# Kernel tuning notes

Hardware: AMD Instinct MI355X
Metric: run time of the kernel (lower is better)

Reference implementation:

```python
import jax, jax.numpy as jnp
import numpy as np

H = 8      # heads
D = 64     # dim_head
N0 = 1024  # modality-0 tokens
N1 = 1024  # modality-1 tokens
N = N0 + N1  # == token_num
DI = H * D   # dim_inner = 512


def setup_inputs() -> dict:
    key = jax.random.key(0)
    ks = jax.random.split(key, 10)
    s = 0.02
    return {
        "x0": jax.random.normal(ks[0], (1, N0, 512), jnp.float32),
        "x1": jax.random.normal(ks[1], (1, N1, 512), jnp.float32),
        "mask0": jnp.ones((1, N0), jnp.bool_),
        "mask1": jnp.ones((1, N1), jnp.bool_),
        "attn_dist": jax.random.normal(ks[2], (1, N, N), jnp.float32),
        "W_in0": jax.random.normal(ks[3], (512, 3 * DI), jnp.float32) * s,
        "W_in1": jax.random.normal(ks[4], (512, 3 * DI), jnp.float32) * s,
        "W_tau": jax.random.normal(ks[5], (DI, N * H), jnp.float32) * s,
        "b_tau": jax.random.normal(ks[6], (N * H,), jnp.float32) * s,
        "W_out0": jax.random.normal(ks[7], (DI, 512), jnp.float32) * s,
        "W_out1": jax.random.normal(ks[8], (DI, 512), jnp.float32) * s,
    }


def _split_heads(qkv, B, n):
    # (B, n, 3*H*D) -> (3, B, H, n, D)   [matches Rearrange 'b n (qkv h d) -> qkv b h n d']
    return qkv.reshape(B, n, 3, H, D).transpose(2, 0, 3, 1, 4)


def reference(x0, x1, mask0, mask1, attn_dist, W_in0, W_in1, W_tau, b_tau, W_out0, W_out1):
    B = x0.shape[0]
    qkv0 = _split_heads(x0 @ W_in0, B, N0)
    qkv1 = _split_heads(x1 @ W_in1, B, N1)
    qkv = jnp.concatenate([qkv0, qkv1], axis=3)  # pack along token axis -> (3,B,H,N,D)
    q, k, v = qkv[0], qkv[1], qkv[2]
    mask = jnp.concatenate([mask0, mask1], axis=1)  # (B, N)

    sim = jnp.einsum('bhid,bhjd->bhij', q, k) / jnp.sqrt(jnp.array(D, q.dtype))
    neg = -jnp.finfo(sim.dtype).max
    sim = jnp.where(mask[:, None, None, :], sim, neg)

    # taus: raw row-major reshape of q (B,H,N,D) -> (B,N,H*D), as in torch .reshape
    q_flat = q.reshape(B, N, H * D)
    taus = (q_flat @ W_tau + b_tau).reshape(B, N, N, H)
    bias = (taus * attn_dist[..., None]).transpose(0, 3, 1, 2)  # (B,H,N,N)
    sim = sim - bias

    attn = jax.nn.softmax(sim.astype(jnp.float32), axis=-1).astype(sim.dtype)
    out = jnp.einsum('bhij,bhjd->bhid', attn, v)
    out = out.transpose(0, 2, 1, 3).reshape(B, N, H * D)  # merge heads

    out0 = out[:, :N0] @ W_out0
    out1 = out[:, N0:] @ W_out1
    return (out0, out1)
```

## Files before the change

### kernel.cpp

```cpp
#include <hip/hip_runtime.h>
#include <stdint.h>

typedef __bf16 bf16;
typedef __bf16 bf16x8 __attribute__((ext_vector_type(8)));
typedef float f32x4 __attribute__((ext_vector_type(4)));
typedef unsigned short u16x8 __attribute__((ext_vector_type(8)));

#define MFMA16(a, b, c) __builtin_amdgcn_mfma_f32_16x16x32_bf16(a, b, c, 0, 0, 0)

static __device__ __forceinline__ bf16x8 lds_frag(const unsigned short* p) {
  return __builtin_bit_cast(bf16x8, *(const u16x8*)p);
}

static __device__ __forceinline__ bf16x8 gmem_frag(const bf16* p) {
  return __builtin_bit_cast(bf16x8, *(const u16x8*)p);
}

static __device__ __forceinline__ u16x8 cvt8(const float* p) {
  f32x4 a = *(const f32x4*)p;
  f32x4 b = *(const f32x4*)(p + 4);
  u16x8 r;
#pragma unroll
  for (int e = 0; e < 4; ++e) {
    r[e] = __builtin_bit_cast(unsigned short, (bf16)a[e]);
    r[4 + e] = __builtin_bit_cast(unsigned short, (bf16)b[e]);
  }
  return r;
}

__global__ __launch_bounds__(256) void prep_kernel(
    const float* __restrict__ Wti, const float* __restrict__ btau,
    const float* __restrict__ x0, const float* __restrict__ x1,
    const float* __restrict__ Win0, const float* __restrict__ Win1,
    const float* __restrict__ Wo0, const float* __restrict__ Wo1,
    bf16* __restrict__ Wto, float* __restrict__ bto, bf16* __restrict__ xb,
    bf16* __restrict__ Winb0, bf16* __restrict__ Winb1,
    bf16* __restrict__ Wob0, bf16* __restrict__ Wob1) {
  const int b = blockIdx.x;
  const int tid = threadIdx.x;
  __shared__ unsigned short shm[8 * 32 * 72];

  if (b < 512) {
    const int c0 = (b & 7) * 64;
    const int j0 = (b >> 3) * 32;
#pragma unroll
    for (int it = 0; it < 8; ++it) {
      int idx = it * 256 + tid;
      int c = idx >> 5, j = idx & 31;
      u16x8 v = cvt8(Wti + (size_t)(c0 + c) * 16384 + (j0 + j) * 8);
#pragma unroll
      for (int h = 0; h < 8; ++h) shm[(h * 32 + j) * 72 + c] = v[h];
    }
    __syncthreads();
#pragma unroll
    for (int it = 0; it < 8; ++it) {
      int chunk = it * 256 + tid;
      int row = chunk >> 3, ck = chunk & 7;
      int h = row >> 5, j = row & 31;
      u16x8 v = *(const u16x8*)&shm[row * 72 + ck * 8];
      *(u16x8*)((unsigned short*)Wto + (size_t)(h * 2048 + j0 + j) * 512 + c0 + ck * 8) = v;
    }
    if ((b & 7) == 0) {
      int j = tid >> 3, h = tid & 7;
      bto[h * 2048 + j0 + j] = btau[(j0 + j) * 8 + h];
    }
  } else if (b < 896) {
    int t = b - 512;
    const float* W = t < 192 ? Win0 : Win1;
    bf16* Wb = t < 192 ? Winb0 : Winb1;
    t = t < 192 ? t : t - 192;
    const int c0 = (t & 7) * 64, n0 = (t >> 3) * 64;
#pragma unroll
    for (int it = 0; it < 2; ++it) {
      int idx = it * 256 + tid;
      int c = idx >> 3, nn = idx & 7;
      u16x8 v = cvt8(W + (size_t)(c0 + c) * 1536 + n0 + nn * 8);
#pragma unroll
      for (int e = 0; e < 8; ++e) shm[(nn * 8 + e) * 72 + c] = v[e];
    }
    __syncthreads();
#pragma unroll
    for (int it = 0; it < 2; ++it) {
      int idx = it * 256 + tid;
      int n = idx >> 3, ck = idx & 7;
      *(u16x8*)((unsigned short*)Wb + (size_t)(n0 + n) * 512 + c0 + ck * 8) =
          *(const u16x8*)&shm[n * 72 + ck * 8];
    }
  } else if (b < 1408) {
    int t = b - 896;
    const float* src = t < 256 ? x0 : x1;
    size_t dst0 = t < 256 ? 0 : 524288;
    int tt = t < 256 ? t : t - 256;
    size_t off = (size_t)tt * 2048 + tid * 8;
    u16x8 v = cvt8(src + off);
    *(u16x8*)((unsigned short*)xb + dst0 + off) = v;
  } else {
    int t = b - 1408;
    const float* W = t < 64 ? Wo0 : Wo1;
    bf16* Wb = t < 64 ? Wob0 : Wob1;
    t &= 63;
    const int c0 = (t & 7) * 64, n0 = (t >> 3) * 64;
#pragma unroll
    for (int it = 0; it < 2; ++it) {
      int idx = it * 256 + tid;
      int c = idx >> 3, nn = idx & 7;
      u16x8 v = cvt8(W + (size_t)(c0 + c) * 512 + n0 + nn * 8);
#pragma unroll
      for (int e = 0; e < 8; ++e) shm[(nn * 8 + e) * 72 + c] = v[e];
    }
    __syncthreads();
#pragma unroll
    for (int it = 0; it < 2; ++it) {
      int idx = it * 256 + tid;
      int n = idx >> 3, ck = idx & 7;
      *(u16x8*)((unsigned short*)Wb + (size_t)(n0 + n) * 512 + c0 + ck * 8) =
          *(const u16x8*)&shm[n * 72 + ck * 8];
    }
  }
}

__global__ __launch_bounds__(256) void qkv_gemm(
    const bf16* __restrict__ xb, const bf16* __restrict__ Winb0, const bf16* __restrict__ Winb1,
    bf16* __restrict__ Qb, bf16* __restrict__ Kb, bf16* __restrict__ Vt_g) {
  const int i0 = blockIdx.x * 128, c0 = blockIdx.y * 128;
  const bf16* Bm = (i0 < 1024) ? Winb0 : Winb1;
  const int tid = threadIdx.x;
  const int lane = tid & 63, wave = tid >> 6;
  const int l16 = lane & 15, quad = lane >> 4;
  const int mrow = (wave & 1) * 64, ncol = (wave >> 1) * 64;
  __shared__ unsigned short As[128 * 64];
  __shared__ unsigned short Bs[128 * 64];
  f32x4 acc[4][4] = {};

  for (int k0 = 0; k0 < 512; k0 += 64) {
    __syncthreads();
#pragma unroll
    for (int c = 0; c < 4; ++c) {
      int s = c * 256 + tid;
      int row = s >> 3, pos = s & 7;
      int kc = pos ^ (row & 7);
      __builtin_amdgcn_global_load_lds((const unsigned int*)(xb + (size_t)(i0 + row) * 512 + k0 + kc * 8),
                                       (unsigned int*)&As[s * 8], 16, 0, 0);
      __builtin_amdgcn_global_load_lds((const unsigned int*)(Bm + (size_t)(c0 + row) * 512 + k0 + kc * 8),
                                       (unsigned int*)&Bs[s * 8], 16, 0, 0);
    }
    __syncthreads();
#pragma unroll
    for (int kb = 0; kb < 2; ++kb) {
      bf16x8 a[4], b[4];
#pragma unroll
      for (int mt = 0; mt < 4; ++mt) {
        int row = mrow + mt * 16 + l16;
        a[mt] = lds_frag(&As[row * 64 + (((kb * 4 + quad) ^ (row & 7)) * 8)]);
      }
#pragma unroll
      for (int nt = 0; nt < 4; ++nt) {
        int row = ncol + nt * 16 + l16;
        b[nt] = lds_frag(&Bs[row * 64 + (((kb * 4 + quad) ^ (row & 7)) * 8)]);
      }
#pragma unroll
      for (int mt = 0; mt < 4; ++mt)
#pragma unroll
        for (int nt = 0; nt < 4; ++nt) acc[mt][nt] = MFMA16(a[mt], b[nt], acc[mt][nt]);
    }
  }
#pragma unroll
  for (int mt = 0; mt < 4; ++mt)
#pragma unroll
    for (int nt = 0; nt < 4; ++nt)
#pragma unroll
      for (int r = 0; r < 4; ++r) {
        int row = i0 + mrow + mt * 16 + quad * 4 + r;
        int col = c0 + ncol + nt * 16 + l16;
        int qsel = col >> 9, h = (col >> 6) & 7, d = col & 63;
        bf16 val = (bf16)acc[mt][nt][r];
        if (qsel == 2) {
          Vt_g[(size_t)(h * 64 + d) * 2048 + row] = val;
        } else {
          bf16* dst = qsel == 0 ? Qb : Kb;
          dst[(size_t)(h * 2048 + row) * 64 + d] = val;
        }
      }
}

__global__ __launch_bounds__(256) void tau_gemm(
    const bf16* __restrict__ Qb, const bf16* __restrict__ Wt,
    const float* __restrict__ bt, const float* __restrict__ ad, bf16* __restrict__ T) {
  const int i0 = blockIdx.x * 128;
  const int j0 = blockIdx.y * 16;
  const int tid = threadIdx.x;
  const int lane = tid & 63, wave = tid >> 6;
  const int l16 = lane & 15, quad = lane >> 4;
  const int mrow = (wave & 1) * 64, ncol = (wave >> 1) * 64;
  __shared__ unsigned short As[128 * 64];
  __shared__ unsigned short Bs[128 * 64];
  f32x4 acc[4][4] = {};

  for (int k0 = 0; k0 < 512; k0 += 64) {
    __syncthreads();
#pragma unroll
    for (int c = 0; c < 4; ++c) {
      int s = c * 256 + tid;
      int row = s >> 3, pos = s & 7;
      int kc = pos ^ (row & 7);
      __builtin_amdgcn_global_load_lds((const unsigned int*)(Qb + (size_t)(i0 + row) * 512 + k0 + kc * 8),
                                       (unsigned int*)&As[s * 8], 16, 0, 0);
      __builtin_amdgcn_global_load_lds(
          (const unsigned int*)(Wt + (size_t)((row >> 4) * 2048 + j0 + (row & 15)) * 512 + k0 + kc * 8),
          (unsigned int*)&Bs[s * 8], 16, 0, 0);
    }
    __syncthreads();
#pragma unroll
    for (int kb = 0; kb < 2; ++kb) {
      bf16x8 a[4], b[4];
#pragma unroll
      for (int mt = 0; mt < 4; ++mt) {
        int row = mrow + mt * 16 + l16;
        a[mt] = lds_frag(&As[row * 64 + (((kb * 4 + quad) ^ (row & 7)) * 8)]);
      }
#pragma unroll
      for (int nt = 0; nt < 4; ++nt) {
        int row = ncol + nt * 16 + l16;
        b[nt] = lds_frag(&Bs[row * 64 + (((kb * 4 + quad) ^ (row & 7)) * 8)]);
      }
#pragma unroll
      for (int mt = 0; mt < 4; ++mt)
#pragma unroll
        for (int nt = 0; nt < 4; ++nt) acc[mt][nt] = MFMA16(a[mt], b[nt], acc[mt][nt]);
    }
  }
  float btv[4];
  int hh[4];
#pragma unroll
  for (int nt = 0; nt < 4; ++nt) {
    int c = ncol + nt * 16 + l16;
    hh[nt] = c >> 4;
    btv[nt] = bt[hh[nt] * 2048 + j0 + l16];
  }
#pragma unroll
  for (int mt = 0; mt < 4; ++mt)
#pragma unroll
    for (int r = 0; r < 4; ++r) {
      int row = i0 + mrow + mt * 16 + quad * 4 + r;
      float av = ad[(size_t)row * 2048 + j0 + l16];
#pragma unroll
      for (int nt = 0; nt < 4; ++nt)
        T[(size_t)hh[nt] * 4194304 + (size_t)row * 2048 + j0 + l16] =
            (bf16)((acc[mt][nt][r] + btv[nt]) * av);
    }
}

__global__ __launch_bounds__(256) void attn_kernel(
    const bf16* __restrict__ Qb, const bf16* __restrict__ Kb, const bf16* __restrict__ Vt_g,
    const bf16* __restrict__ T, float* __restrict__ Op, float* __restrict__ Ml) {
  const int h = blockIdx.y;
  const int i0 = blockIdx.x * 64;
  const int js = blockIdx.z;
  const int tid = threadIdx.x;
  const int lane = tid & 63, wave = tid >> 6;
  const int l16 = lane & 15, quad = lane >> 4;
  __shared__ unsigned short Ks[64 * 64];
  __shared__ unsigned short Vt[64 * 64];
  __shared__ unsigned short Tb[64 * 64];
  __shared__ unsigned short Ps[64 * 72];

  const bf16* Kh = Kb + (size_t)h * (2048 * 64);
  const bf16* Vh = Vt_g + (size_t)h * (64 * 2048);
  const bf16* Th = T + (size_t)h * (2048 * 2048);

  bf16x8 aQ[2];
#pragma unroll
  for (int kk = 0; kk < 2; ++kk)
    aQ[kk] = gmem_frag(Qb + (size_t)(h * 2048 + i0 + wave * 16 + l16) * 64 + kk * 32 + quad * 8);
  f32x4 Oacc[4] = {};
  float m_run[4], l_run[4];
#pragma unroll
  for (int r = 0; r < 4; ++r) { m_run[r] = -3.0e38f; l_run[r] = 0.f; }
  const int rowl = wave * 16 + quad * 4;

  for (int t = 0; t < 8; ++t) {
    const int j0 = js * 512 + t * 64;
    __syncthreads();
#pragma unroll
    for (int c = 0; c < 2; ++c) {
      int s = c * 256 + tid;
      int r8 = s >> 3, pos = s & 7;
      int sc = pos ^ (r8 & 7);
      __builtin_amdgcn_global_load_lds(
          (const unsigned int*)(Kh + (size_t)(j0 + r8) * 64 + sc * 8),
          (unsigned int*)&Ks[s * 8], 16, 0, 0);
      __builtin_amdgcn_global_load_lds(
          (const unsigned int*)(Vh + (size_t)r8 * 2048 + j0 + sc * 8),
          (unsigned int*)&Vt[s * 8], 16, 0, 0);
      __builtin_amdgcn_global_load_lds(
          (const unsigned int*)(Th + (size_t)(i0 + r8) * 2048 + j0 + pos * 8),
          (unsigned int*)&Tb[s * 8], 16, 0, 0);
    }
    __syncthreads();

    f32x4 S[4] = {};
#pragma unroll
    for (int nt = 0; nt < 4; ++nt) {
      int row = nt * 16 + l16;
#pragma unroll
      for (int kk = 0; kk < 2; ++kk) {
        bf16x8 bk = lds_frag(&Ks[row * 64 + (((kk * 4 + quad) ^ (row & 7)) * 8)]);
        S[nt] = MFMA16(aQ[kk], bk, S[nt]);
      }
    }
    float sv[4][4];
#pragma unroll
    for (int nt = 0; nt < 4; ++nt)
#pragma unroll
      for (int r = 0; r < 4; ++r) {
        float tb = (float)__builtin_bit_cast(bf16, Tb[(rowl + r) * 64 + nt * 16 + l16]);
        sv[nt][r] = S[nt][r] * 0.125f - tb;
      }
#pragma unroll
    for (int r = 0; r < 4; ++r) {
      float mx = fmaxf(fmaxf(sv[0][r], sv[1][r]), fmaxf(sv[2][r], sv[3][r]));
#pragma unroll
      for (int o = 1; o < 16; o <<= 1) mx = fmaxf(mx, __shfl_xor(mx, o, 16));
      float mnew = fmaxf(m_run[r], mx);
      float alpha = __expf(m_run[r] - mnew);
      m_run[r] = mnew;
      float rs = 0.f;
#pragma unroll
      for (int nt = 0; nt < 4; ++nt) { sv[nt][r] = __expf(sv[nt][r] - mnew); rs += sv[nt][r]; }
#pragma unroll
      for (int o = 1; o < 16; o <<= 1) rs += __shfl_xor(rs, o, 16);
      l_run[r] = l_run[r] * alpha + rs;
#pragma unroll
      for (int dt = 0; dt < 4; ++dt) Oacc[dt][r] *= alpha;
    }
#pragma unroll
    for (int nt = 0; nt < 4; ++nt)
#pragma unroll
      for (int r = 0; r < 4; ++r)
        Ps[(rowl + r) * 72 + nt * 16 + l16] =
            __builtin_bit_cast(unsigned short, (bf16)sv[nt][r]);
    __builtin_amdgcn_s_waitcnt(0xC07F);
    __builtin_amdgcn_wave_barrier();
#pragma unroll
    for (int kk = 0; kk < 2; ++kk) {
      bf16x8 aP = lds_frag(&Ps[(wave * 16 + l16) * 72 + kk * 32 + quad * 8]);
#pragma unroll
      for (int dt = 0; dt < 4; ++dt) {
        int row = dt * 16 + l16;
        bf16x8 bv = lds_frag(&Vt[row * 64 + (((kk * 4 + quad) ^ (row & 7)) * 8)]);
        Oacc[dt] = MFMA16(aP, bv, Oacc[dt]);
      }
    }
    __builtin_amdgcn_wave_barrier();
  }
  const size_t pb = ((size_t)js * 8 + h) * 2048;
#pragma unroll
  for (int r = 0; r < 4; ++r) {
    int rowg = i0 + rowl + r;
#pragma unroll
    for (int dt = 0; dt < 4; ++dt)
      Op[(pb + rowg) * 64 + dt * 16 + l16] = Oacc[dt][r];
    if (l16 == 0) {
      Ml[(pb + rowg) * 2 + 0] = m_run[r];
      Ml[(pb + rowg) * 2 + 1] = l_run[r];
    }
  }
}

__global__ __launch_bounds__(256) void merge_kernel(
    const float* __restrict__ Op, const float* __restrict__ Ml, bf16* __restrict__ om) {
  const int gr = blockIdx.x * 4 + (threadIdx.x >> 6);
  const int d = threadIdx.x & 63;
  float ms[4];
  float mmax = -3.0e38f;
#pragma unroll
  for (int s = 0; s < 4; ++s) {
    ms[s] = Ml[((size_t)s * 16384 + gr) * 2 + 0];
    mmax = fmaxf(mmax, ms[s]);
  }
  float lsum = 0.f, o = 0.f;
#pragma unroll
  for (int s = 0; s < 4; ++s) {
    float w = __expf(ms[s] - mmax);
    lsum += Ml[((size_t)s * 16384 + gr) * 2 + 1] * w;
    o += Op[((size_t)s * 16384 + gr) * 64 + d] * w;
  }
  int h = gr >> 11, i = gr & 2047;
  om[(size_t)i * 512 + h * 64 + d] = (bf16)(o / lsum);
}

__global__ __launch_bounds__(256) void out_proj(
    const bf16* __restrict__ om, const bf16* __restrict__ Wob0, const bf16* __restrict__ Wob1,
    float* __restrict__ out) {
  const int mod = blockIdx.z;
  const bf16* Bw = mod ? Wob1 : Wob0;
  float* outp = out + (size_t)mod * (1024 * 512);
  const int i0 = blockIdx.x * 64, c0 = blockIdx.y * 64;
  const int grow0 = mod * 1024 + i0;
  const int tid = threadIdx.x;
  const int lane = tid & 63, wave = tid >> 6;
  const int l16 = lane & 15, quad = lane >> 4;
  const int mrow = (wave & 1) * 32, ncol = (wave >> 1) * 32;
  __shared__ unsigned short As[64 * 64];
  __shared__ unsigned short Bs[64 * 64];
  f32x4 acc[2][2] = {};

  for (int k0 = 0; k0 < 512; k0 += 64) {
    __syncthreads();
#pragma unroll
    for (int c = 0; c < 2; ++c) {
      int s = c * 256 + tid;
      int row = s >> 3, pos = s & 7;
      int kc = pos ^ (row & 7);
      __builtin_amdgcn_global_load_lds((const unsigned int*)(om + (size_t)(grow0 + row) * 512 + k0 + kc * 8),
                                       (unsigned int*)&As[s * 8], 16, 0, 0);
      __builtin_amdgcn_global_load_lds((const unsigned int*)(Bw + (size_t)(c0 + row) * 512 + k0 + kc * 8),
                                       (unsigned int*)&Bs[s * 8], 16, 0, 0);
    }
    __syncthreads();
#pragma unroll
    for (int kb = 0; kb < 2; ++kb) {
      bf16x8 a[2], b[2];
#pragma unroll
      for (int mt = 0; mt < 2; ++mt) {
        int row = mrow + mt * 16 + l16;
        a[mt] = lds_frag(&As[row * 64 + (((kb * 4 + quad) ^ (row & 7)) * 8)]);
      }
#pragma unroll
      for (int nt = 0; nt < 2; ++nt) {
        int row = ncol + nt * 16 + l16;
        b[nt] = lds_frag(&Bs[row * 64 + (((kb * 4 + quad) ^ (row & 7)) * 8)]);
      }
#pragma unroll
      for (int mt = 0; mt < 2; ++mt)
#pragma unroll
        for (int nt = 0; nt < 2; ++nt) acc[mt][nt] = MFMA16(a[mt], b[nt], acc[mt][nt]);
    }
  }
#pragma unroll
  for (int mt = 0; mt < 2; ++mt)
#pragma unroll
    for (int nt = 0; nt < 2; ++nt)
#pragma unroll
      for (int r = 0; r < 4; ++r) {
        int row = i0 + mrow + mt * 16 + quad * 4 + r;
        int col = c0 + ncol + nt * 16 + l16;
        outp[(size_t)row * 512 + col] = acc[mt][nt][r];
      }
}

extern "C" void kernel_launch(void* const* d_in, const int* in_sizes, int n_in,
                              void* d_out, int out_size, void* d_ws, size_t ws_size,
                              hipStream_t stream) {
  (void)in_sizes; (void)n_in; (void)out_size; (void)ws_size;
  const float* x0   = (const float*)d_in[0];
  const float* x1   = (const float*)d_in[1];
  const float* ad   = (const float*)d_in[4];
  const float* Win0 = (const float*)d_in[5];
  const float* Win1 = (const float*)d_in[6];
  const float* Wtau = (const float*)d_in[7];
  const float* btau = (const float*)d_in[8];
  const float* Wo0  = (const float*)d_in[9];
  const float* Wo1  = (const float*)d_in[10];
  float* out = (float*)d_out;

  bf16* ws = (bf16*)d_ws;
  bf16* Qb = ws;
  bf16* Kb = Qb + 1048576;
  bf16* Vt_g = Kb + 1048576;
  bf16* Wt = Vt_g + 1048576;
  bf16* T  = Wt + 8388608;
  bf16* om = T + 33554432;
  float* bt = (float*)(om + 1048576);
  float* Ml = bt + 16384;
  bf16* Wob0 = (bf16*)(Ml + 131072);
  bf16* Wob1 = Wob0 + 262144;
  float* Op = (float*)Wt;
  bf16* xb    = T;
  bf16* Winb0 = T + 1048576;
  bf16* Winb1 = Winb0 + 786432;

  prep_kernel<<<1536, 256, 0, stream>>>(Wtau, btau, x0, x1, Win0, Win1, Wo0, Wo1,
                                        Wt, bt, xb, Winb0, Winb1, Wob0, Wob1);
  qkv_gemm<<<dim3(16, 12), 256, 0, stream>>>(xb, Winb0, Winb1, Qb, Kb, Vt_g);
  tau_gemm<<<dim3(16, 128), 256, 0, stream>>>(Qb, Wt, bt, ad, T);
  attn_kernel<<<dim3(32, 8, 4), 256, 0, stream>>>(Qb, Kb, Vt_g, T, Op, Ml);
  merge_kernel<<<4096, 256, 0, stream>>>(Op, Ml, om);
  out_proj<<<dim3(16, 8, 2), 256, 0, stream>>>(om, Wob0, Wob1, out);
}
```

Measured before the change: 237.5 us.

## Fuse tau bias GEMM into flash attention kernel, dropping the T intermediate

Removes the separate tau_gemm, which wrote a 64 MB bf16 bias tensor T that the attention kernel then read back. The fused kernel computes the per-head tau tile (Q_flat x Wt slice) on the fly in each 64-wide key tile, applies the bias and the attn_dist scaling in registers, then runs the online softmax. Each block now covers 128 query rows with two 16-row subtiles per wave. The aim is to cut the large HBM write and read of T, at the cost of an inner K-loop GEMM with extra LDS traffic and syncs inside every attention tile, plus fewer blocks (512).

```diff
diff --git a/kernel.cpp b/kernel.cpp
--- a/kernel.cpp
+++ b/kernel.cpp
@@ -183,100 +183,43 @@
       }
 }
 
-__global__ __launch_bounds__(256) void tau_gemm(
-    const bf16* __restrict__ Qb, const bf16* __restrict__ Wt,
-    const float* __restrict__ bt, const float* __restrict__ ad, bf16* __restrict__ T) {
+__global__ __launch_bounds__(256) void fused_attn(
+    const bf16* __restrict__ Qb, const bf16* __restrict__ Kb, const bf16* __restrict__ Vt_g,
+    const bf16* __restrict__ Wt, const float* __restrict__ bt, const float* __restrict__ ad,
+    float* __restrict__ Op, float* __restrict__ Ml) {
+  const int h = blockIdx.y;
   const int i0 = blockIdx.x * 128;
-  const int j0 = blockIdx.y * 16;
-  const int tid = threadIdx.x;
-  const int lane = tid & 63, wave = tid >> 6;
-  const int l16 = lane & 15, quad = lane >> 4;
-  const int mrow = (wave & 1) * 64, ncol = (wave >> 1) * 64;
-  __shared__ unsigned short As[128 * 64];
-  __shared__ unsigned short Bs[128 * 64];
-  f32x4 acc[4][4] = {};
-
-  for (int k0 = 0; k0 < 512; k0 += 64) {
-    __syncthreads();
-#pragma unroll
-    for (int c = 0; c < 4; ++c) {
-      int s = c * 256 + tid;
-      int row = s >> 3, pos = s & 7;
-      int kc = pos ^ (row & 7);
-      __builtin_amdgcn_global_load_lds((const unsigned int*)(Qb + (size_t)(i0 + row) * 512 + k0 + kc * 8),
-                                       (unsigned int*)&As[s * 8], 16, 0, 0);
-      __builtin_amdgcn_global_load_lds(
-          (const unsigned int*)(Wt + (size_t)((row >> 4) * 2048 + j0 + (row & 15)) * 512 + k0 + kc * 8),
-          (unsigned int*)&Bs[s * 8], 16, 0, 0);
-    }
-    __syncthreads();
-#pragma unroll
-    for (int kb = 0; kb < 2; ++kb) {
-      bf16x8 a[4], b[4];
-#pragma unroll
-      for (int mt = 0; mt < 4; ++mt) {
-        int row = mrow + mt * 16 + l16;
-        a[mt] = lds_frag(&As[row * 64 + (((kb * 4 + quad) ^ (row & 7)) * 8)]);
-      }
-#pragma unroll
-      for (int nt = 0; nt < 4; ++nt) {
-        int row = ncol + nt * 16 + l16;
-        b[nt] = lds_frag(&Bs[row * 64 + (((kb * 4 + quad) ^ (row & 7)) * 8)]);
-      }
-#pragma unroll
-      for (int mt = 0; mt < 4; ++mt)
-#pragma unroll
-        for (int nt = 0; nt < 4; ++nt) acc[mt][nt] = MFMA16(a[mt], b[nt], acc[mt][nt]);
-    }
-  }
-  float btv[4];
-  int hh[4];
-#pragma unroll
-  for (int nt = 0; nt < 4; ++nt) {
-    int c = ncol + nt * 16 + l16;
-    hh[nt] = c >> 4;
-    btv[nt] = bt[hh[nt] * 2048 + j0 + l16];
-  }
-#pragma unroll
-  for (int mt = 0; mt < 4; ++mt)
-#pragma unroll
-    for (int r = 0; r < 4; ++r) {
-      int row = i0 + mrow + mt * 16 + quad * 4 + r;
-      float av = ad[(size_t)row * 2048 + j0 + l16];
-#pragma unroll
-      for (int nt = 0; nt < 4; ++nt)
-        T[(size_t)hh[nt] * 4194304 + (size_t)row * 2048 + j0 + l16] =
-            (bf16)((acc[mt][nt][r] + btv[nt]) * av);
-    }
-}
-
-__global__ __launch_bounds__(256) void attn_kernel(
-    const bf16* __restrict__ Qb, const bf16* __restrict__ Kb, const bf16* __restrict__ Vt_g,
-    const bf16* __restrict__ T, float* __restrict__ Op, float* __restrict__ Ml) {
-  const int h = blockIdx.y;
-  const int i0 = blockIdx.x * 64;
   const int js = blockIdx.z;
   const int tid = threadIdx.x;
   const int lane = tid & 63, wave = tid >> 6;
   const int l16 = lane & 15, quad = lane >> 4;
+  const int wrow = wave * 32;
+  const int rq = quad * 4;
+
+  __shared__ unsigned short As[128 * 64];
+  __shared__ unsigned short Bs[64 * 64];
   __shared__ unsigned short Ks[64 * 64];
   __shared__ unsigned short Vt[64 * 64];
-  __shared__ unsigned short Tb[64 * 64];
-  __shared__ unsigned short Ps[64 * 72];
+  __shared__ unsigned short Ps[128 * 72];
 
   const bf16* Kh = Kb + (size_t)h * (2048 * 64);
   const bf16* Vh = Vt_g + (size_t)h * (64 * 2048);
-  const bf16* Th = T + (size_t)h * (2048 * 2048);
-
-  bf16x8 aQ[2];
-#pragma unroll
-  for (int kk = 0; kk < 2; ++kk)
-    aQ[kk] = gmem_frag(Qb + (size_t)(h * 2048 + i0 + wave * 16 + l16) * 64 + kk * 32 + quad * 8);
-  f32x4 Oacc[4] = {};
-  float m_run[4], l_run[4];
-#pragma unroll
-  for (int r = 0; r < 4; ++r) { m_run[r] = -3.0e38f; l_run[r] = 0.f; }
-  const int rowl = wave * 16 + quad * 4;
+  const bf16* Wh = Wt + (size_t)h * 2048 * 512;
+
+  bf16x8 aQh[2][2];
+#pragma unroll
+  for (int mt = 0; mt < 2; ++mt)
+#pragma unroll
+    for (int kk = 0; kk < 2; ++kk)
+      aQh[mt][kk] = gmem_frag(Qb + (size_t)(h * 2048 + i0 + wrow + mt * 16 + l16) * 64 +
+                              kk * 32 + quad * 8);
+
+  f32x4 Oacc[2][4] = {};
+  float m_run[2][4], l_run[2][4];
+#pragma unroll
+  for (int mt = 0; mt < 2; ++mt)
+#pragma unroll
+    for (int r = 0; r < 4; ++r) { m_run[mt][r] = -3.0e38f; l_run[mt][r] = 0.f; }
 
   for (int t = 0; t < 8; ++t) {
     const int j0 = js * 512 + t * 64;
@@ -292,79 +235,130 @@
       __builtin_amdgcn_global_load_lds(
           (const unsigned int*)(Vh + (size_t)r8 * 2048 + j0 + sc * 8),
           (unsigned int*)&Vt[s * 8], 16, 0, 0);
-      __builtin_amdgcn_global_load_lds(
-          (const unsigned int*)(Th + (size_t)(i0 + r8) * 2048 + j0 + pos * 8),
-          (unsigned int*)&Tb[s * 8], 16, 0, 0);
-    }
-    __syncthreads();
-
-    f32x4 S[4] = {};
+    }
+
+    f32x4 acc[2][4] = {};
+    for (int k0 = 0; k0 < 512; k0 += 64) {
+      if (k0) __syncthreads();
+#pragma unroll
+      for (int c = 0; c < 4; ++c) {
+        int s = c * 256 + tid;
+        int row = s >> 3, pos = s & 7;
+        int kc = pos ^ (row & 7);
+        __builtin_amdgcn_global_load_lds(
+            (const unsigned int*)(Qb + (size_t)(i0 + row) * 512 + k0 + kc * 8),
+            (unsigned int*)&As[s * 8], 16, 0, 0);
+      }
+#pragma unroll
+      for (int c = 0; c < 2; ++c) {
+        int s = c * 256 + tid;
+        int row = s >> 3, pos = s & 7;
+        int kc = pos ^ (row & 7);
+        __builtin_amdgcn_global_load_lds(
+            (const unsigned int*)(Wh + (size_t)(j0 + row) * 512 + k0 + kc * 8),
+            (unsigned int*)&Bs[s * 8], 16, 0, 0);
+      }
+      __syncthreads();
+#pragma unroll
+      for (int kb = 0; kb < 2; ++kb) {
+        bf16x8 a[2], b[4];
+#pragma unroll
+        for (int mt = 0; mt < 2; ++mt) {
+          int row = wrow + mt * 16 + l16;
+          a[mt] = lds_frag(&As[row * 64 + (((kb * 4 + quad) ^ (row & 7)) * 8)]);
+        }
+#pragma unroll
+        for (int nt = 0; nt < 4; ++nt) {
+          int row = nt * 16 + l16;
+          b[nt] = lds_frag(&Bs[row * 64 + (((kb * 4 + quad) ^ (row & 7)) * 8)]);
+        }
+#pragma unroll
+        for (int mt = 0; mt < 2; ++mt)
+#pragma unroll
+          for (int nt = 0; nt < 4; ++nt) acc[mt][nt] = MFMA16(a[mt], b[nt], acc[mt][nt]);
+      }
+    }
+
+    f32x4 S[2][4] = {};
 #pragma unroll
     for (int nt = 0; nt < 4; ++nt) {
-      int row = nt * 16 + l16;
+      int krow = nt * 16 + l16;
 #pragma unroll
       for (int kk = 0; kk < 2; ++kk) {
-        bf16x8 bk = lds_frag(&Ks[row * 64 + (((kk * 4 + quad) ^ (row & 7)) * 8)]);
-        S[nt] = MFMA16(aQ[kk], bk, S[nt]);
-      }
-    }
-    float sv[4][4];
-#pragma unroll
-    for (int nt = 0; nt < 4; ++nt)
+        bf16x8 bk = lds_frag(&Ks[krow * 64 + (((kk * 4 + quad) ^ (krow & 7)) * 8)]);
+        S[0][nt] = MFMA16(aQh[0][kk], bk, S[0][nt]);
+        S[1][nt] = MFMA16(aQh[1][kk], bk, S[1][nt]);
+      }
+    }
+
+    float btv[4];
+#pragma unroll
+    for (int nt = 0; nt < 4; ++nt) btv[nt] = bt[h * 2048 + j0 + nt * 16 + l16];
+#pragma unroll
+    for (int mt = 0; mt < 2; ++mt) {
+      float sv[4][4];
+#pragma unroll
+      for (int nt = 0; nt < 4; ++nt)
+#pragma unroll
+        for (int r = 0; r < 4; ++r) {
+          float av = ad[(size_t)(i0 + wrow + mt * 16 + rq + r) * 2048 + j0 + nt * 16 + l16];
+          sv[nt][r] = S[mt][nt][r] * 0.125f - (acc[mt][nt][r] + btv[nt]) * av;
+        }
 #pragma unroll
       for (int r = 0; r < 4; ++r) {
-        float tb = (float)__builtin_bit_cast(bf16, Tb[(rowl + r) * 64 + nt * 16 + l16]);
-        sv[nt][r] = S[nt][r] * 0.125f - tb;
-      }
-#pragma unroll
-    for (int r = 0; r < 4; ++r) {
-      float mx = fmaxf(fmaxf(sv[0][r], sv[1][r]), fmaxf(sv[2][r], sv[3][r]));
-#pragma unroll
-      for (int o = 1; o < 16; o <<= 1) mx = fmaxf(mx, __shfl_xor(mx, o, 16));
-      float mnew = fmaxf(m_run[r], mx);
-      float alpha = __expf(m_run[r] - mnew);
-      m_run[r] = mnew;
-      float rs = 0.f;
-#pragma unroll
-      for (int nt = 0; nt < 4; ++nt) { sv[nt][r] = __expf(sv[nt][r] - mnew); rs += sv[nt][r]; }
-#pragma unroll
-      for (int o = 1; o < 16; o <<= 1) rs += __shfl_xor(rs, o, 16);
-      l_run[r] = l_run[r] * alpha + rs;
-#pragma unroll
-      for (int dt = 0; dt < 4; ++dt) Oacc[dt][r] *= alpha;
-    }
-#pragma unroll
-    for (int nt = 0; nt < 4; ++nt)
-#pragma unroll
-      for (int r = 0; r < 4; ++r)
-        Ps[(rowl + r) * 72 + nt * 16 + l16] =
-            __builtin_bit_cast(unsigned short, (bf16)sv[nt][r]);
+        float mx = fmaxf(fmaxf(sv[0][r], sv[1][r]), fmaxf(sv[2][r], sv[3][r]));
+#pragma unroll
+        for (int o = 1; o < 16; o <<= 1) mx = fmaxf(mx, __shfl_xor(mx, o, 16));
+        float mnew = fmaxf(m_run[mt][r], mx);
+        float alpha = __expf(m_run[mt][r] - mnew);
+        m_run[mt][r] = mnew;
+        float rs = 0.f;
+#pragma unroll
+        for (int nt = 0; nt < 4; ++nt) { sv[nt][r] = __expf(sv[nt][r] - mnew); rs += sv[nt][r]; }
+#pragma unroll
+        for (int o = 1; o < 16; o <<= 1) rs += __shfl_xor(rs, o, 16);
+        l_run[mt][r] = l_run[mt][r] * alpha + rs;
+#pragma unroll
+        for (int dt = 0; dt < 4; ++dt) Oacc[mt][dt][r] *= alpha;
+      }
+#pragma unroll
+      for (int nt = 0; nt < 4; ++nt)
+#pragma unroll
+        for (int r = 0; r < 4; ++r)
+          Ps[(wrow + mt * 16 + rq + r) * 72 + nt * 16 + l16] =
+              __builtin_bit_cast(unsigned short, (bf16)sv[nt][r]);
+    }
     __builtin_amdgcn_s_waitcnt(0xC07F);
     __builtin_amdgcn_wave_barrier();
 #pragma unroll
     for (int kk = 0; kk < 2; ++kk) {
-      bf16x8 aP = lds_frag(&Ps[(wave * 16 + l16) * 72 + kk * 32 + quad * 8]);
+      bf16x8 aP0 = lds_frag(&Ps[(wrow + l16) * 72 + kk * 32 + quad * 8]);
+      bf16x8 aP1 = lds_frag(&Ps[(wrow + 16 + l16) * 72 + kk * 32 + quad * 8]);
 #pragma unroll
       for (int dt = 0; dt < 4; ++dt) {
-        int row = dt * 16 + l16;
-        bf16x8 bv = lds_frag(&Vt[row * 64 + (((kk * 4 + quad) ^ (row & 7)) * 8)]);
-        Oacc[dt] = MFMA16(aP, bv, Oacc[dt]);
+        int vrow = dt * 16 + l16;
+        bf16x8 bv = lds_frag(&Vt[vrow * 64 + (((kk * 4 + quad) ^ (vrow & 7)) * 8)]);
+        Oacc[0][dt] = MFMA16(aP0, bv, Oacc[0][dt]);
+        Oacc[1][dt] = MFMA16(aP1, bv, Oacc[1][dt]);
       }
     }
     __builtin_amdgcn_wave_barrier();
   }
+
   const size_t pb = ((size_t)js * 8 + h) * 2048;
 #pragma unroll
-  for (int r = 0; r < 4; ++r) {
-    int rowg = i0 + rowl + r;
-#pragma unroll
-    for (int dt = 0; dt < 4; ++dt)
-      Op[(pb + rowg) * 64 + dt * 16 + l16] = Oacc[dt][r];
-    if (l16 == 0) {
-      Ml[(pb + rowg) * 2 + 0] = m_run[r];
-      Ml[(pb + rowg) * 2 + 1] = l_run[r];
-    }
-  }
+  for (int mt = 0; mt < 2; ++mt)
+#pragma unroll
+    for (int r = 0; r < 4; ++r) {
+      int rowg = i0 + wrow + mt * 16 + rq + r;
+#pragma unroll
+      for (int dt = 0; dt < 4; ++dt)
+        Op[(pb + rowg) * 64 + dt * 16 + l16] = Oacc[mt][dt][r];
+      if (l16 == 0) {
+        Ml[(pb + rowg) * 2 + 0] = m_run[mt][r];
+        Ml[(pb + rowg) * 2 + 1] = l_run[mt][r];
+      }
+    }
 }
 
 __global__ __launch_bounds__(256) void merge_kernel(
@@ -475,16 +469,15 @@
   float* Ml = bt + 16384;
   bf16* Wob0 = (bf16*)(Ml + 131072);
   bf16* Wob1 = Wob0 + 262144;
-  float* Op = (float*)Wt;
   bf16* xb    = T;
   bf16* Winb0 = T + 1048576;
   bf16* Winb1 = Winb0 + 786432;
+  float* Op = (float*)T;
 
   prep_kernel<<<1536, 256, 0, stream>>>(Wtau, btau, x0, x1, Win0, Win1, Wo0, Wo1,
                                         Wt, bt, xb, Winb0, Winb1, Wob0, Wob1);
   qkv_gemm<<<dim3(16, 12), 256, 0, stream>>>(xb, Winb0, Winb1, Qb, Kb, Vt_g);
-  tau_gemm<<<dim3(16, 128), 256, 0, stream>>>(Qb, Wt, bt, ad, T);
-  attn_kernel<<<dim3(32, 8, 4), 256, 0, stream>>>(Qb, Kb, Vt_g, T, Op, Ml);
+  fused_attn<<<dim3(16, 8, 4), 256, 0, stream>>>(Qb, Kb, Vt_g, Wt, bt, ad, Op, Ml);
   merge_kernel<<<4096, 256, 0, stream>>>(Op, Ml, om);
   out_proj<<<dim3(16, 8, 2), 256, 0, stream>>>(om, Wob0, Wob1, out);
 }
```

New measurement: 280.7 us. 18.2% more time.
